# Kernel tuning notes

Hardware: AMD Instinct MI355X
Metric: run time of the kernel (lower is better)

Reference implementation:

```python
import jax, jax.numpy as jnp
import numpy as np

N, IN_F, OUT_F = 4096, 4096, 4096
THRESH = 0.05


def setup_inputs() -> dict:
    key = jax.random.key(0)
    k_x, k_w = jax.random.split(key)
    last_out = jax.random.normal(k_x, (N, IN_F), dtype=jnp.float32)
    # learned weight buffer, [out_features, in_features] like torch Linear
    weight = jax.random.normal(k_w, (OUT_F, IN_F), dtype=jnp.float32) * (1.0 / np.sqrt(IN_F))
    threshold = jnp.float32(THRESH)
    return {"last_out": last_out, "weight": weight, "threshold": threshold}


def reference(last_out, weight, threshold):
    # rtp_linear: runtime threshold pruning — activations with |x| <= threshold
    # are skipped (treated as zero) in the matmul. Bias buffer is unused
    # (dead code in the original forward).
    x = jnp.where(jnp.abs(last_out) > threshold, last_out, 0.0)
    # y[n, o] = sum_i x[n, i] * W[o, i]
    return jnp.einsum("ni,oi->no", x, weight)
```

## Files before the change

kernel.cpp:

```cpp
#include <hip/hip_runtime.h>
#include <hip/hip_bf16.h>

#define M_DIM 4096
#define N_DIM 4096
#define K_DIM 4096

typedef __attribute__((ext_vector_type(8))) __bf16 bf16x8;
typedef __attribute__((ext_vector_type(8))) short short8;
typedef __attribute__((ext_vector_type(8))) unsigned short ushort8;
typedef __attribute__((ext_vector_type(4))) float f32x4;

__device__ __forceinline__ void gload_lds16(const void* g, void* l) {
    __builtin_amdgcn_global_load_lds(
        (const __attribute__((address_space(1))) void*)g,
        (__attribute__((address_space(3))) void*)l,
        16, 0, 0);
}

__device__ __forceinline__ bf16x8 ld8(const unsigned short* p) {
    short8 r = *reinterpret_cast<const short8*>(p);
    return __builtin_bit_cast(bf16x8, r);
}

__global__ void prune_cvt2(const float* __restrict__ x,
                           const float* __restrict__ w,
                           unsigned short* __restrict__ xb,
                           unsigned short* __restrict__ wb,
                           const float* __restrict__ thrp, int n8) {
    const float thr = thrp[0];
    const int stride = gridDim.x * blockDim.x;
    const int total = 2 * n8;
    for (int idx = blockIdx.x * blockDim.x + threadIdx.x; idx < total; idx += stride) {
        const bool isx = idx < n8;
        const int j = isx ? idx : idx - n8;
        const float* src = isx ? x : w;
        unsigned short* dst = isx ? xb : wb;
        const float te = isx ? thr : -1.0f;
        const float4* p = reinterpret_cast<const float4*>(src) + 2 * (size_t)j;
        float4 v0 = p[0];
        float4 v1 = p[1];
        float v[8] = {v0.x, v0.y, v0.z, v0.w, v1.x, v1.y, v1.z, v1.w};
        ushort8 o;
#pragma unroll
        for (int e = 0; e < 8; ++e) {
            float f = v[e];
            f = (fabsf(f) > te) ? f : 0.0f;
            __hip_bfloat16 hh = __float2bfloat16(f);
            o[e] = *reinterpret_cast<unsigned short*>(&hh);
        }
        *reinterpret_cast<ushort8*>(dst + 8 * (size_t)j) = o;
    }
}

__global__ __launch_bounds__(512, 2) void gemm_8phase(
        const unsigned short* __restrict__ A,
        const unsigned short* __restrict__ B,
        float* __restrict__ C) {
    __shared__ __align__(16) unsigned short lds[65536];

    const int tid  = threadIdx.x;
    const int lane = tid & 63;
    const int wid  = tid >> 6;
    const int wr   = wid >> 2;
    const int wc   = wid & 3;

    const int bid = blockIdx.x;
    const int swz = (bid & 7) * 32 + (bid >> 3);
    const int bm = (swz >> 4) * 256;
    const int bn = (swz & 15) * 256;

    const int g  = tid & 255;
    const int ah = tid >> 8;
    const int arow = bm + ah * 128 + (g >> 3);
    const int acol = 8 * ((g & 7) ^ ((g >> 3) & 7));
    const unsigned short* Asrc = A + (size_t)arow * K_DIM + acol;
    const int AdstE = ah * 8192 + g * 8;

    const int h = lane + 64 * wr;
    const int brow = bn + wc * 64 + (h >> 3);
    const int bcol = 8 * ((h & 7) ^ ((h >> 3) & 7));
    const unsigned short* Bsrc = B + (size_t)brow * K_DIM + bcol;
    const int BdstE = wc * 4096 + h * 8;

#define SA(dstb, j, kg) gload_lds16(Asrc + (size_t)(32*(j))*K_DIM + (kg), (dstb) + AdstE + 2048*(j))
#define SB(dstb, j, kg) gload_lds16(Bsrc + (size_t)(16*(j))*K_DIM + (kg), (dstb) + BdstE + 1024*(j))

    const int fr  = lane & 15;
    const int kq4 = lane >> 4;
    const int rowOffA = (wr * 128 + fr) * 64;
    const int rowOffB = (wc * 64 + fr) * 64;
    const int sk0 = 8 * ((kq4    ) ^ (fr & 7));
    const int sk1 = 8 * ((kq4 + 4) ^ (fr & 7));

    f32x4 acc[8][4] = {};

    bf16x8 bfr[4][2];
#define MFMA16(q, A00, A10, A01, A11)                                                              \
    __builtin_amdgcn_s_setprio(1);                                                                 \
    _Pragma("unroll")                                                                              \
    for (int n = 0; n < 4; ++n) {                                                                  \
        acc[2*(q)][n]   = __builtin_amdgcn_mfma_f32_16x16x32_bf16(A00, bfr[n][0], acc[2*(q)][n], 0, 0, 0);   \
        acc[2*(q)+1][n] = __builtin_amdgcn_mfma_f32_16x16x32_bf16(A10, bfr[n][0], acc[2*(q)+1][n], 0, 0, 0); \
    }                                                                                              \
    _Pragma("unroll")                                                                              \
    for (int n = 0; n < 4; ++n) {                                                                  \
        acc[2*(q)][n]   = __builtin_amdgcn_mfma_f32_16x16x32_bf16(A01, bfr[n][1], acc[2*(q)][n], 0, 0, 0);   \
        acc[2*(q)+1][n] = __builtin_amdgcn_mfma_f32_16x16x32_bf16(A11, bfr[n][1], acc[2*(q)+1][n], 0, 0, 0); \
    }                                                                                              \
    __builtin_amdgcn_s_setprio(0);

    SB(lds + 32768, 0, 0); SB(lds + 32768, 1, 0); SB(lds + 32768, 2, 0); SB(lds + 32768, 3, 0);
    SA(lds,         0, 0); SA(lds,         1, 0); SA(lds,         2, 0); SA(lds,         3, 0);
    asm volatile("s_waitcnt vmcnt(2)" ::: "memory");
    asm volatile("s_barrier" ::: "memory");

    bf16x8 p00 = ld8(lds + rowOffA + 0 * 1024 + sk0);
    bf16x8 p10 = ld8(lds + rowOffA + 1 * 1024 + sk0);
    bf16x8 p01 = ld8(lds + rowOffA + 0 * 1024 + sk1);
    bf16x8 p11 = ld8(lds + rowOffA + 1 * 1024 + sk1);

    for (int t = 0; t < 64; ++t) {
        const int cur = t & 1, nxt = cur ^ 1;
        const unsigned short* Ab  = lds + cur * 16384;
        const unsigned short* Bb  = lds + 32768 + cur * 16384;
        unsigned short* AbN = lds + nxt * 16384;
        unsigned short* BbN = lds + 32768 + nxt * 16384;
        const unsigned short* AbNr = AbN;
        const int kn = (t < 63 ? t + 1 : 63) * 64;

        {
#pragma unroll
            for (int n = 0; n < 4; ++n) {
                bfr[n][0] = ld8(Bb + rowOffB + n * 1024 + sk0);
                bfr[n][1] = ld8(Bb + rowOffB + n * 1024 + sk1);
            }
            bf16x8 q00 = ld8(Ab + rowOffA + 2 * 1024 + sk0);
            bf16x8 q10 = ld8(Ab + rowOffA + 3 * 1024 + sk0);
            bf16x8 q01 = ld8(Ab + rowOffA + 2 * 1024 + sk1);
            bf16x8 q11 = ld8(Ab + rowOffA + 3 * 1024 + sk1);
            SB(BbN, 0, kn); SB(BbN, 1, kn); SB(BbN, 2, kn); SB(BbN, 3, kn);
            MFMA16(0, p00, p10, p01, p11);
            asm volatile("s_waitcnt vmcnt(5)" ::: "memory");
            asm volatile("s_barrier" ::: "memory");

            bf16x8 r00 = ld8(Ab + rowOffA + 4 * 1024 + sk0);
            bf16x8 r10 = ld8(Ab + rowOffA + 5 * 1024 + sk0);
            bf16x8 r01 = ld8(Ab + rowOffA + 4 * 1024 + sk1);
            bf16x8 r11 = ld8(Ab + rowOffA + 5 * 1024 + sk1);
            SA(AbN, 0, kn); SA(AbN, 1, kn);
            MFMA16(1, q00, q10, q01, q11);
            asm volatile("s_waitcnt vmcnt(6)" ::: "memory");
            asm volatile("s_barrier" ::: "memory");

            bf16x8 s00 = ld8(Ab + rowOffA + 6 * 1024 + sk0);
            bf16x8 s10 = ld8(Ab + rowOffA + 7 * 1024 + sk0);
            bf16x8 s01 = ld8(Ab + rowOffA + 6 * 1024 + sk1);
            bf16x8 s11 = ld8(Ab + rowOffA + 7 * 1024 + sk1);
            SA(AbN, 2, kn); SA(AbN, 3, kn);
            MFMA16(2, r00, r10, r01, r11);
            asm volatile("s_waitcnt vmcnt(3)" ::: "memory");
            asm volatile("s_barrier" ::: "memory");

            p00 = ld8(AbNr + rowOffA + 0 * 1024 + sk0);
            p10 = ld8(AbNr + rowOffA + 1 * 1024 + sk0);
            p01 = ld8(AbNr + rowOffA + 0 * 1024 + sk1);
            p11 = ld8(AbNr + rowOffA + 1 * 1024 + sk1);
            MFMA16(3, s00, s10, s01, s11);
            asm volatile("s_waitcnt vmcnt(2)" ::: "memory");
            asm volatile("s_barrier" ::: "memory");
        }
    }

    asm volatile("s_waitcnt vmcnt(0)" ::: "memory");

    const int crow = bm + wr * 128 + kq4 * 4;
    const int ccol = bn + wc * 64 + fr;
#pragma unroll
    for (int m = 0; m < 8; ++m)
#pragma unroll
        for (int n = 0; n < 4; ++n)
#pragma unroll
            for (int j = 0; j < 4; ++j)
                C[(size_t)(crow + m * 16 + j) * N_DIM + ccol + n * 16] = acc[m][n][j];
}

__global__ void gemm_f32_fallback(const float* __restrict__ A,
                                  const float* __restrict__ B,
                                  float* __restrict__ C,
                                  const float* __restrict__ thrp) {
    __shared__ float As[32][33];
    __shared__ float Bs[32][33];
    const float thr = thrp[0];
    const int tx = threadIdx.x, ty = threadIdx.y;
    const int row = blockIdx.y * 32 + ty;
    float acc = 0.0f;
    for (int k0 = 0; k0 < K_DIM; k0 += 32) {
        float a = A[(size_t)row * K_DIM + k0 + tx];
        As[ty][tx] = (fabsf(a) > thr) ? a : 0.0f;
        Bs[ty][tx] = B[(size_t)(blockIdx.x * 32 + ty) * K_DIM + k0 + tx];
        __syncthreads();
#pragma unroll 8
        for (int kk = 0; kk < 32; ++kk)
            acc += As[ty][kk] * Bs[tx][kk];
        __syncthreads();
    }
    C[(size_t)row * N_DIM + blockIdx.x * 32 + tx] = acc;
}

extern "C" void kernel_launch(void* const* d_in, const int* in_sizes, int n_in,
                              void* d_out, int out_size, void* d_ws, size_t ws_size,
                              hipStream_t stream) {
    const float* x    = (const float*)d_in[0];
    const float* w    = (const float*)d_in[1];
    const float* thrp = (const float*)d_in[2];
    float* out = (float*)d_out;

    const size_t elems = (size_t)M_DIM * K_DIM;
    if (ws_size >= 2 * elems * sizeof(unsigned short)) {
        unsigned short* Ab = (unsigned short*)d_ws;
        unsigned short* Bb = Ab + elems;
        const int n8 = (int)(elems / 8);
        prune_cvt2<<<2048, 256, 0, stream>>>(x, w, Ab, Bb, thrp, n8);
        gemm_8phase<<<dim3(256), dim3(512), 0, stream>>>(Ab, Bb, out);
    } else {
        dim3 grid(N_DIM / 32, M_DIM / 32), blk(32, 32);
        gemm_f32_fallback<<<grid, blk, 0, stream>>>(x, w, out, thrp);
    }
}
```

Measured before the change: 146.4 us.

## Restructure GEMM main loop into k-half phases with B prefetched two tiles ahead

Reorganises the bf16 MFMA main loop so each phase multiplies four A fragments by four B fragments for one 32-wide k-half, instead of interleaving per-row-pair groups. The B tile is now prefetched two k-steps ahead into the buffer just consumed, and the A tile one step ahead, with revised waitcnt/barrier placement. The aim is to spread LDS reads and global-to-LDS copies more evenly across MFMA phases and reduce stalls. The two-ahead B schedule and the reused buffers are fragile, so a mistake in the waitcnt counts could race or serialise the pipeline.

```diff
diff --git a/kernel.cpp b/kernel.cpp
--- a/kernel.cpp
+++ b/kernel.cpp
@@ -94,81 +94,91 @@
 
     f32x4 acc[8][4] = {};
 
-    bf16x8 bfr[4][2];
-#define MFMA16(q, A00, A10, A01, A11)                                                              \
-    __builtin_amdgcn_s_setprio(1);                                                                 \
-    _Pragma("unroll")                                                                              \
-    for (int n = 0; n < 4; ++n) {                                                                  \
-        acc[2*(q)][n]   = __builtin_amdgcn_mfma_f32_16x16x32_bf16(A00, bfr[n][0], acc[2*(q)][n], 0, 0, 0);   \
-        acc[2*(q)+1][n] = __builtin_amdgcn_mfma_f32_16x16x32_bf16(A10, bfr[n][0], acc[2*(q)+1][n], 0, 0, 0); \
-    }                                                                                              \
-    _Pragma("unroll")                                                                              \
-    for (int n = 0; n < 4; ++n) {                                                                  \
-        acc[2*(q)][n]   = __builtin_amdgcn_mfma_f32_16x16x32_bf16(A01, bfr[n][1], acc[2*(q)][n], 0, 0, 0);   \
-        acc[2*(q)+1][n] = __builtin_amdgcn_mfma_f32_16x16x32_bf16(A11, bfr[n][1], acc[2*(q)+1][n], 0, 0, 0); \
-    }                                                                                              \
-    __builtin_amdgcn_s_setprio(0);
+    bf16x8 aA0, aA1, aA2, aA3;
+    bf16x8 aB0, aB1, aB2, aB3;
+    bf16x8 b00, b01, b02, b03;
+    bf16x8 b10, b11, b12, b13;
+
+#define PH_MFMA(q, S0, S1, S2, S3, T0, T1, T2, T3)                              \
+    {                                                                           \
+        __builtin_amdgcn_s_setprio(1);                                          \
+        const bf16x8 Aq_[4] = {S0, S1, S2, S3};                                 \
+        const bf16x8 Bq_[4] = {T0, T1, T2, T3};                                 \
+        _Pragma("unroll")                                                       \
+        for (int i_ = 0; i_ < 4; ++i_)                                          \
+            _Pragma("unroll")                                                   \
+            for (int n_ = 0; n_ < 4; ++n_)                                      \
+                acc[4*(q)+i_][n_] = __builtin_amdgcn_mfma_f32_16x16x32_bf16(    \
+                    Aq_[i_], Bq_[n_], acc[4*(q)+i_][n_], 0, 0, 0);              \
+        __builtin_amdgcn_s_setprio(0);                                          \
+    }
 
     SB(lds + 32768, 0, 0); SB(lds + 32768, 1, 0); SB(lds + 32768, 2, 0); SB(lds + 32768, 3, 0);
     SA(lds,         0, 0); SA(lds,         1, 0); SA(lds,         2, 0); SA(lds,         3, 0);
-    asm volatile("s_waitcnt vmcnt(2)" ::: "memory");
+    SB(lds + 49152, 0, 64); SB(lds + 49152, 1, 64); SB(lds + 49152, 2, 64); SB(lds + 49152, 3, 64);
+    asm volatile("s_waitcnt vmcnt(4)" ::: "memory");
     asm volatile("s_barrier" ::: "memory");
 
-    bf16x8 p00 = ld8(lds + rowOffA + 0 * 1024 + sk0);
-    bf16x8 p10 = ld8(lds + rowOffA + 1 * 1024 + sk0);
-    bf16x8 p01 = ld8(lds + rowOffA + 0 * 1024 + sk1);
-    bf16x8 p11 = ld8(lds + rowOffA + 1 * 1024 + sk1);
+    aA0 = ld8(lds + rowOffA + 0 * 1024 + sk0);
+    aA1 = ld8(lds + rowOffA + 1 * 1024 + sk0);
+    aA2 = ld8(lds + rowOffA + 2 * 1024 + sk0);
+    aA3 = ld8(lds + rowOffA + 3 * 1024 + sk0);
+    b00 = ld8(lds + 32768 + rowOffB + 0 * 1024 + sk0);
+    b01 = ld8(lds + 32768 + rowOffB + 1 * 1024 + sk0);
+    b02 = ld8(lds + 32768 + rowOffB + 2 * 1024 + sk0);
+    b03 = ld8(lds + 32768 + rowOffB + 3 * 1024 + sk0);
 
     for (int t = 0; t < 64; ++t) {
         const int cur = t & 1, nxt = cur ^ 1;
-        const unsigned short* Ab  = lds + cur * 16384;
-        const unsigned short* Bb  = lds + 32768 + cur * 16384;
-        unsigned short* AbN = lds + nxt * 16384;
-        unsigned short* BbN = lds + 32768 + nxt * 16384;
-        const unsigned short* AbNr = AbN;
-        const int kn = (t < 63 ? t + 1 : 63) * 64;
-
-        {
-#pragma unroll
-            for (int n = 0; n < 4; ++n) {
-                bfr[n][0] = ld8(Bb + rowOffB + n * 1024 + sk0);
-                bfr[n][1] = ld8(Bb + rowOffB + n * 1024 + sk1);
-            }
-            bf16x8 q00 = ld8(Ab + rowOffA + 2 * 1024 + sk0);
-            bf16x8 q10 = ld8(Ab + rowOffA + 3 * 1024 + sk0);
-            bf16x8 q01 = ld8(Ab + rowOffA + 2 * 1024 + sk1);
-            bf16x8 q11 = ld8(Ab + rowOffA + 3 * 1024 + sk1);
-            SB(BbN, 0, kn); SB(BbN, 1, kn); SB(BbN, 2, kn); SB(BbN, 3, kn);
-            MFMA16(0, p00, p10, p01, p11);
-            asm volatile("s_waitcnt vmcnt(5)" ::: "memory");
-            asm volatile("s_barrier" ::: "memory");
-
-            bf16x8 r00 = ld8(Ab + rowOffA + 4 * 1024 + sk0);
-            bf16x8 r10 = ld8(Ab + rowOffA + 5 * 1024 + sk0);
-            bf16x8 r01 = ld8(Ab + rowOffA + 4 * 1024 + sk1);
-            bf16x8 r11 = ld8(Ab + rowOffA + 5 * 1024 + sk1);
-            SA(AbN, 0, kn); SA(AbN, 1, kn);
-            MFMA16(1, q00, q10, q01, q11);
-            asm volatile("s_waitcnt vmcnt(6)" ::: "memory");
-            asm volatile("s_barrier" ::: "memory");
-
-            bf16x8 s00 = ld8(Ab + rowOffA + 6 * 1024 + sk0);
-            bf16x8 s10 = ld8(Ab + rowOffA + 7 * 1024 + sk0);
-            bf16x8 s01 = ld8(Ab + rowOffA + 6 * 1024 + sk1);
-            bf16x8 s11 = ld8(Ab + rowOffA + 7 * 1024 + sk1);
-            SA(AbN, 2, kn); SA(AbN, 3, kn);
-            MFMA16(2, r00, r10, r01, r11);
-            asm volatile("s_waitcnt vmcnt(3)" ::: "memory");
-            asm volatile("s_barrier" ::: "memory");
-
-            p00 = ld8(AbNr + rowOffA + 0 * 1024 + sk0);
-            p10 = ld8(AbNr + rowOffA + 1 * 1024 + sk0);
-            p01 = ld8(AbNr + rowOffA + 0 * 1024 + sk1);
-            p11 = ld8(AbNr + rowOffA + 1 * 1024 + sk1);
-            MFMA16(3, s00, s10, s01, s11);
-            asm volatile("s_waitcnt vmcnt(2)" ::: "memory");
-            asm volatile("s_barrier" ::: "memory");
-        }
+        const unsigned short* Ab   = lds + cur * 16384;
+        const unsigned short* AbNr = lds + nxt * 16384;
+        unsigned short*       AbN  = lds + nxt * 16384;
+        const unsigned short* Bb   = lds + 32768 + cur * 16384;
+        const unsigned short* BbNr = lds + 32768 + nxt * 16384;
+        unsigned short*       BbC  = lds + 32768 + cur * 16384;
+        const int kna = (t < 63 ? t + 1 : 63) * 64;
+        const int knb = (t < 62 ? t + 2 : 63) * 64;
+
+        aB0 = ld8(Ab + rowOffA + 4 * 1024 + sk0);
+        aB1 = ld8(Ab + rowOffA + 5 * 1024 + sk0);
+        aB2 = ld8(Ab + rowOffA + 6 * 1024 + sk0);
+        aB3 = ld8(Ab + rowOffA + 7 * 1024 + sk0);
+        b10 = ld8(Bb + rowOffB + 0 * 1024 + sk1);
+        b11 = ld8(Bb + rowOffB + 1 * 1024 + sk1);
+        PH_MFMA(0, aA0, aA1, aA2, aA3, b00, b01, b02, b03);
+        asm volatile("s_barrier" ::: "memory");
+
+        aA0 = ld8(Ab + rowOffA + 0 * 1024 + sk1);
+        aA1 = ld8(Ab + rowOffA + 1 * 1024 + sk1);
+        aA2 = ld8(Ab + rowOffA + 2 * 1024 + sk1);
+        aA3 = ld8(Ab + rowOffA + 3 * 1024 + sk1);
+        b12 = ld8(Bb + rowOffB + 2 * 1024 + sk1);
+        b13 = ld8(Bb + rowOffB + 3 * 1024 + sk1);
+        SA(AbN, 0, kna); SA(AbN, 1, kna); SA(AbN, 2, kna); SA(AbN, 3, kna);
+        PH_MFMA(1, aB0, aB1, aB2, aB3, b00, b01, b02, b03);
+        asm volatile("s_waitcnt vmcnt(4)" ::: "memory");
+        asm volatile("s_barrier" ::: "memory");
+
+        aB0 = ld8(Ab + rowOffA + 4 * 1024 + sk1);
+        aB1 = ld8(Ab + rowOffA + 5 * 1024 + sk1);
+        aB2 = ld8(Ab + rowOffA + 6 * 1024 + sk1);
+        aB3 = ld8(Ab + rowOffA + 7 * 1024 + sk1);
+        b00 = ld8(BbNr + rowOffB + 0 * 1024 + sk0);
+        b01 = ld8(BbNr + rowOffB + 1 * 1024 + sk0);
+        PH_MFMA(0, aA0, aA1, aA2, aA3, b10, b11, b12, b13);
+        asm volatile("s_waitcnt vmcnt(2)" ::: "memory");
+        asm volatile("s_barrier" ::: "memory");
+
+        aA0 = ld8(AbNr + rowOffA + 0 * 1024 + sk0);
+        aA1 = ld8(AbNr + rowOffA + 1 * 1024 + sk0);
+        aA2 = ld8(AbNr + rowOffA + 2 * 1024 + sk0);
+        aA3 = ld8(AbNr + rowOffA + 3 * 1024 + sk0);
+        b02 = ld8(BbNr + rowOffB + 2 * 1024 + sk0);
+        b03 = ld8(BbNr + rowOffB + 3 * 1024 + sk0);
+        SB(BbC, 0, knb); SB(BbC, 1, knb); SB(BbC, 2, knb); SB(BbC, 3, knb);
+        PH_MFMA(1, aB0, aB1, aB2, aB3, b10, b11, b12, b13);
+        asm volatile("s_waitcnt vmcnt(4)" ::: "memory");
+        asm volatile("s_barrier" ::: "memory");
     }
 
     asm volatile("s_waitcnt vmcnt(0)" ::: "memory");
```

Measured after the change: 148.2 us. No clear change (+1.3%).

## Restructure GEMM main loop into four k-half phases with 4x4 MFMA blocks

Applied to the files above, without the earlier changes.

Reorganizes the inner loop of the bf16 MFMA GEMM. Each tile step now runs four phases that split the 64-wide k slice into two halves and the A rows into two groups, and each phase issues a 4x4 block of MFMAs over freshly loaded A and B fragments. The old version prefetched the next A fragments across barriers and held all B fragments for the whole step. The new schedule holds fewer fragment registers and interleaves the global-to-LDS prefetches differently. In exchange it adds explicit lgkmcnt(0) waits and extra barriers per phase, so LDS read latency is exposed before each MFMA group instead of overlapping with the previous one.

```diff
diff --git a/kernel.cpp b/kernel.cpp
--- a/kernel.cpp
+++ b/kernel.cpp
@@ -93,20 +93,20 @@
     const int sk1 = 8 * ((kq4 + 4) ^ (fr & 7));
 
     f32x4 acc[8][4] = {};
-
-    bf16x8 bfr[4][2];
-#define MFMA16(q, A00, A10, A01, A11)                                                              \
-    __builtin_amdgcn_s_setprio(1);                                                                 \
-    _Pragma("unroll")                                                                              \
-    for (int n = 0; n < 4; ++n) {                                                                  \
-        acc[2*(q)][n]   = __builtin_amdgcn_mfma_f32_16x16x32_bf16(A00, bfr[n][0], acc[2*(q)][n], 0, 0, 0);   \
-        acc[2*(q)+1][n] = __builtin_amdgcn_mfma_f32_16x16x32_bf16(A10, bfr[n][0], acc[2*(q)+1][n], 0, 0, 0); \
-    }                                                                                              \
-    _Pragma("unroll")                                                                              \
-    for (int n = 0; n < 4; ++n) {                                                                  \
-        acc[2*(q)][n]   = __builtin_amdgcn_mfma_f32_16x16x32_bf16(A01, bfr[n][1], acc[2*(q)][n], 0, 0, 0);   \
-        acc[2*(q)+1][n] = __builtin_amdgcn_mfma_f32_16x16x32_bf16(A11, bfr[n][1], acc[2*(q)+1][n], 0, 0, 0); \
-    }                                                                                              \
+    bf16x8 a0, a1, a2, a3, b0, b1, b2, b3;
+
+#define MFMA_PH(base)                                                           \
+    __builtin_amdgcn_s_setprio(1);                                              \
+    {                                                                           \
+        const bf16x8 Av_[4] = {a0, a1, a2, a3};                                 \
+        const bf16x8 Bv_[4] = {b0, b1, b2, b3};                                 \
+        _Pragma("unroll")                                                       \
+        for (int i_ = 0; i_ < 4; ++i_)                                          \
+            _Pragma("unroll")                                                   \
+            for (int n_ = 0; n_ < 4; ++n_)                                      \
+                acc[4*(base)+i_][n_] = __builtin_amdgcn_mfma_f32_16x16x32_bf16( \
+                    Av_[i_], Bv_[n_], acc[4*(base)+i_][n_], 0, 0, 0);           \
+    }                                                                           \
     __builtin_amdgcn_s_setprio(0);
 
     SB(lds + 32768, 0, 0); SB(lds + 32768, 1, 0); SB(lds + 32768, 2, 0); SB(lds + 32768, 3, 0);
@@ -114,61 +114,63 @@
     asm volatile("s_waitcnt vmcnt(2)" ::: "memory");
     asm volatile("s_barrier" ::: "memory");
 
-    bf16x8 p00 = ld8(lds + rowOffA + 0 * 1024 + sk0);
-    bf16x8 p10 = ld8(lds + rowOffA + 1 * 1024 + sk0);
-    bf16x8 p01 = ld8(lds + rowOffA + 0 * 1024 + sk1);
-    bf16x8 p11 = ld8(lds + rowOffA + 1 * 1024 + sk1);
-
     for (int t = 0; t < 64; ++t) {
         const int cur = t & 1, nxt = cur ^ 1;
-        const unsigned short* Ab  = lds + cur * 16384;
-        const unsigned short* Bb  = lds + 32768 + cur * 16384;
+        const unsigned short* Ab = lds + cur * 16384;
+        const unsigned short* Bb = lds + 32768 + cur * 16384;
         unsigned short* AbN = lds + nxt * 16384;
         unsigned short* BbN = lds + 32768 + nxt * 16384;
-        const unsigned short* AbNr = AbN;
         const int kn = (t < 63 ? t + 1 : 63) * 64;
 
-        {
-#pragma unroll
-            for (int n = 0; n < 4; ++n) {
-                bfr[n][0] = ld8(Bb + rowOffB + n * 1024 + sk0);
-                bfr[n][1] = ld8(Bb + rowOffB + n * 1024 + sk1);
-            }
-            bf16x8 q00 = ld8(Ab + rowOffA + 2 * 1024 + sk0);
-            bf16x8 q10 = ld8(Ab + rowOffA + 3 * 1024 + sk0);
-            bf16x8 q01 = ld8(Ab + rowOffA + 2 * 1024 + sk1);
-            bf16x8 q11 = ld8(Ab + rowOffA + 3 * 1024 + sk1);
-            SB(BbN, 0, kn); SB(BbN, 1, kn); SB(BbN, 2, kn); SB(BbN, 3, kn);
-            MFMA16(0, p00, p10, p01, p11);
-            asm volatile("s_waitcnt vmcnt(5)" ::: "memory");
-            asm volatile("s_barrier" ::: "memory");
-
-            bf16x8 r00 = ld8(Ab + rowOffA + 4 * 1024 + sk0);
-            bf16x8 r10 = ld8(Ab + rowOffA + 5 * 1024 + sk0);
-            bf16x8 r01 = ld8(Ab + rowOffA + 4 * 1024 + sk1);
-            bf16x8 r11 = ld8(Ab + rowOffA + 5 * 1024 + sk1);
-            SA(AbN, 0, kn); SA(AbN, 1, kn);
-            MFMA16(1, q00, q10, q01, q11);
-            asm volatile("s_waitcnt vmcnt(6)" ::: "memory");
-            asm volatile("s_barrier" ::: "memory");
-
-            bf16x8 s00 = ld8(Ab + rowOffA + 6 * 1024 + sk0);
-            bf16x8 s10 = ld8(Ab + rowOffA + 7 * 1024 + sk0);
-            bf16x8 s01 = ld8(Ab + rowOffA + 6 * 1024 + sk1);
-            bf16x8 s11 = ld8(Ab + rowOffA + 7 * 1024 + sk1);
-            SA(AbN, 2, kn); SA(AbN, 3, kn);
-            MFMA16(2, r00, r10, r01, r11);
-            asm volatile("s_waitcnt vmcnt(3)" ::: "memory");
-            asm volatile("s_barrier" ::: "memory");
-
-            p00 = ld8(AbNr + rowOffA + 0 * 1024 + sk0);
-            p10 = ld8(AbNr + rowOffA + 1 * 1024 + sk0);
-            p01 = ld8(AbNr + rowOffA + 0 * 1024 + sk1);
-            p11 = ld8(AbNr + rowOffA + 1 * 1024 + sk1);
-            MFMA16(3, s00, s10, s01, s11);
-            asm volatile("s_waitcnt vmcnt(2)" ::: "memory");
-            asm volatile("s_barrier" ::: "memory");
-        }
+        b0 = ld8(Bb + rowOffB + 0 * 1024 + sk0);
+        b1 = ld8(Bb + rowOffB + 1 * 1024 + sk0);
+        b2 = ld8(Bb + rowOffB + 2 * 1024 + sk0);
+        b3 = ld8(Bb + rowOffB + 3 * 1024 + sk0);
+        a0 = ld8(Ab + rowOffA + 0 * 1024 + sk0);
+        a1 = ld8(Ab + rowOffA + 1 * 1024 + sk0);
+        a2 = ld8(Ab + rowOffA + 2 * 1024 + sk0);
+        a3 = ld8(Ab + rowOffA + 3 * 1024 + sk0);
+        SB(BbN, 0, kn); SB(BbN, 1, kn);
+        asm volatile("s_barrier" ::: "memory");
+        asm volatile("s_waitcnt lgkmcnt(0)" ::: "memory");
+        MFMA_PH(0);
+        asm volatile("s_waitcnt vmcnt(2)" ::: "memory");
+        asm volatile("s_barrier" ::: "memory");
+
+        a0 = ld8(Ab + rowOffA + 4 * 1024 + sk0);
+        a1 = ld8(Ab + rowOffA + 5 * 1024 + sk0);
+        a2 = ld8(Ab + rowOffA + 6 * 1024 + sk0);
+        a3 = ld8(Ab + rowOffA + 7 * 1024 + sk0);
+        SB(BbN, 2, kn); SB(BbN, 3, kn);
+        asm volatile("s_barrier" ::: "memory");
+        asm volatile("s_waitcnt lgkmcnt(0)" ::: "memory");
+        MFMA_PH(1);
+        asm volatile("s_barrier" ::: "memory");
+
+        b0 = ld8(Bb + rowOffB + 0 * 1024 + sk1);
+        b1 = ld8(Bb + rowOffB + 1 * 1024 + sk1);
+        b2 = ld8(Bb + rowOffB + 2 * 1024 + sk1);
+        b3 = ld8(Bb + rowOffB + 3 * 1024 + sk1);
+        a0 = ld8(Ab + rowOffA + 0 * 1024 + sk1);
+        a1 = ld8(Ab + rowOffA + 1 * 1024 + sk1);
+        a2 = ld8(Ab + rowOffA + 2 * 1024 + sk1);
+        a3 = ld8(Ab + rowOffA + 3 * 1024 + sk1);
+        SA(AbN, 0, kn); SA(AbN, 1, kn);
+        asm volatile("s_barrier" ::: "memory");
+        asm volatile("s_waitcnt lgkmcnt(0)" ::: "memory");
+        MFMA_PH(0);
+        asm volatile("s_barrier" ::: "memory");
+
+        a0 = ld8(Ab + rowOffA + 4 * 1024 + sk1);
+        a1 = ld8(Ab + rowOffA + 5 * 1024 + sk1);
+        a2 = ld8(Ab + rowOffA + 6 * 1024 + sk1);
+        a3 = ld8(Ab + rowOffA + 7 * 1024 + sk1);
+        SA(AbN, 2, kn); SA(AbN, 3, kn);
+        asm volatile("s_barrier" ::: "memory");
+        asm volatile("s_waitcnt lgkmcnt(0)" ::: "memory");
+        MFMA_PH(1);
+        asm volatile("s_waitcnt vmcnt(2)" ::: "memory");
+        asm volatile("s_barrier" ::: "memory");
     }
 
     asm volatile("s_waitcnt vmcnt(0)" ::: "memory");
```

Measured after the change: 153.4 us. 1.05x slower.
